# Performance work log

Measured on AMD Instinct MI355X. Metric: run time of the kernel, lower is better.

Reference implementation:

```python
import jax, jax.numpy as jnp
import numpy as np

L_SEQ = 2048
RECEPTIVE = 128  # band half-width
B, H, D = 2, 16, 64


def _band_mask(l, r, dtype):
    i = jnp.arange(l)
    return (jnp.abs(i[:, None] - i[None, :]) <= r).astype(dtype)


def setup_inputs() -> dict:
    key = jax.random.key(0)
    kq, kk = jax.random.split(key)
    queries = jax.random.normal(kq, (B, H, L_SEQ, D), dtype=jnp.float32)
    keys = jax.random.normal(kk, (B, H, L_SEQ, D), dtype=jnp.float32)
    return {"queries": queries, "keys": keys}


def reference(queries, keys):
    # Original: sum_d( q[...,i,None,d] * mask[i,j] * k[...,None,j,d] )
    # Mask is independent of d, so this equals (Q @ K^T) * band_mask.
    band = _band_mask(queries.shape[-2], RECEPTIVE, queries.dtype)  # [L, L]
    scores = jnp.einsum('bhid,bhjd->bhij', queries, keys)  # [B, H, L, L]
    return scores * band
```

## Files before the change

kernel.cpp:

```cpp
#include <hip/hip_runtime.h>


constexpr int L = 2048;
constexpr int D = 64;
constexpr int R = 128;
constexpr int TILE = 64;
constexpr int NT = L / TILE;

__global__ __launch_bounds__(256, 4)
void receptive_attention_kernel(const float* __restrict__ q,
                                const float* __restrict__ k,
                                float* __restrict__ out) {
    const int ti = blockIdx.x;
    const int y  = blockIdx.y;
    const int bh = blockIdx.z;
    const int t  = threadIdx.x;

    const int kind = (y & 1) ? (5 + (y >> 1)) : (y >> 1);

    const int jt_lo = (ti - 2 > 0) ? (ti - 2) : 0;
    const int jt_hi = (ti + 2 < NT - 1) ? (ti + 2) : (NT - 1);

    float* outStrip = out + (size_t)bh * L * L + (size_t)ti * TILE * L;

    if (kind >= 5) {
        const int r0  = (kind - 5) * 16;
        const int wl4 = (jt_lo * TILE) / 4;
        const int rb  = (jt_hi + 1) * TILE;
        const int nz4 = (L - (jt_hi - jt_lo + 1) * TILE) / 4;
        const float4 z = make_float4(0.f, 0.f, 0.f, 0.f);
        for (int r = 0; r < 16; ++r) {
            float* orow = outStrip + (size_t)(r0 + r) * L;
            for (int f = t; f < nz4; f += 256) {
                int col = (f < wl4) ? (f * 4) : (rb + (f - wl4) * 4);
                *reinterpret_cast<float4*>(orow + col) = z;
            }
        }
        return;
    }

    const int tj = ti + kind - 2;
    if (tj < 0 || tj >= NT) return;

    __shared__ __align__(16) float Qs[TILE * 64];
    __shared__ __align__(16) float Ks[TILE * 64];

    const float* qTile = q + ((size_t)bh * L + (size_t)ti * TILE) * D;
    const float* kTile = k + ((size_t)bh * L + (size_t)tj * TILE) * D;

    #pragma unroll
    for (int it = 0; it < 4; ++it) {
        int idx  = t + it * 256;
        int row  = idx >> 4;
        int col4 = idx & 15;
        float4 qv = *reinterpret_cast<const float4*>(qTile + row * D + col4 * 4);
        float4 kv = *reinterpret_cast<const float4*>(kTile + row * D + col4 * 4);
        int wblk = (col4 ^ (row >> 2)) & 15;
        *reinterpret_cast<float4*>(&Qs[row * 64 + wblk * 4]) = qv;
        *reinterpret_cast<float4*>(&Ks[row * 64 + wblk * 4]) = kv;
    }
    __syncthreads();

    const int tr = (t >> 4) * 4;
    const int tc = (t & 15) * 4;
    const int xq = (t >> 4) & 15;
    const int xk = t & 15;

    float acc[4][4] = {};
    #pragma unroll 4
    for (int b = 0; b < 16; ++b) {
        float4 qv[4], kv[4];
        const int qb = ((b ^ xq) & 15) * 4;
        const int kb = ((b ^ xk) & 15) * 4;
        #pragma unroll
        for (int r = 0; r < 4; ++r)
            qv[r] = *reinterpret_cast<const float4*>(&Qs[(tr + r) * 64 + qb]);
        #pragma unroll
        for (int c = 0; c < 4; ++c)
            kv[c] = *reinterpret_cast<const float4*>(&Ks[(tc + c) * 64 + kb]);
        #pragma unroll
        for (int rr = 0; rr < 4; ++rr) {
            #pragma unroll
            for (int cc = 0; cc < 4; ++cc) {
                acc[rr][cc] += qv[rr].x * kv[cc].x;
                acc[rr][cc] += qv[rr].y * kv[cc].y;
                acc[rr][cc] += qv[rr].z * kv[cc].z;
                acc[rr][cc] += qv[rr].w * kv[cc].w;
            }
        }
    }

    float* outTile = outStrip + tj * TILE;
    const int gi0 = ti * TILE + tr;
    const int gj0 = tj * TILE + tc;
    #pragma unroll
    for (int rr = 0; rr < 4; ++rr) {
        int gi = gi0 + rr;
        float4 v;
        float* vp = &v.x;
        #pragma unroll
        for (int cc = 0; cc < 4; ++cc) {
            int gj = gj0 + cc;
            int diff = gi - gj;
            if (diff < 0) diff = -diff;
            vp[cc] = (diff <= R) ? acc[rr][cc] : 0.f;
        }
        *reinterpret_cast<float4*>(outTile + (size_t)(tr + rr) * L + tc) = v;
    }
}

extern "C" void kernel_launch(void* const* d_in, const int* in_sizes, int n_in,
                              void* d_out, int out_size, void* d_ws, size_t ws_size,
                              hipStream_t stream) {
    const float* q = (const float*)d_in[0];
    const float* k = (const float*)d_in[1];
    float* out = (float*)d_out;

    dim3 grid(NT, 9, 32);
    receptive_attention_kernel<<<grid, 256, 0, stream>>>(q, k, out);
}
```

Measured before the change: 552.5 us.

## Merge band tiles and zero-fill into one block per row strip

Each block now handles a full 64-row output strip. It loads Q once and two warpgroups compute up to five K tiles, with K prefetched from registers into shared memory. Band results are staged in shared memory so every thread writes full-row float4 stores that cover both band and zero regions. This removes the separate zero-fill blocks and the repeated Q loads, in exchange for more syncs, higher register pressure from three accumulator sets, and a 48KB shared arena.

```diff
diff --git a/kernel.cpp b/kernel.cpp
--- a/kernel.cpp
+++ b/kernel.cpp
@@ -6,106 +6,155 @@
 constexpr int R = 128;
 constexpr int TILE = 64;
 constexpr int NT = L / TILE;
+constexpr int ARENA = 3 * TILE * 64;
 
-__global__ __launch_bounds__(256, 4)
+__global__ __launch_bounds__(512, 4)
 void receptive_attention_kernel(const float* __restrict__ q,
                                 const float* __restrict__ k,
                                 float* __restrict__ out) {
     const int ti = blockIdx.x;
-    const int y  = blockIdx.y;
-    const int bh = blockIdx.z;
+    const int bh = blockIdx.y;
     const int t  = threadIdx.x;
-
-    const int kind = (y & 1) ? (5 + (y >> 1)) : (y >> 1);
 
     const int jt_lo = (ti - 2 > 0) ? (ti - 2) : 0;
     const int jt_hi = (ti + 2 < NT - 1) ? (ti + 2) : (NT - 1);
+    const int ntj   = jt_hi - jt_lo + 1;
+    const int c0    = jt_lo * TILE;
 
-    float* outStrip = out + (size_t)bh * L * L + (size_t)ti * TILE * L;
-
-    if (kind >= 5) {
-        const int r0  = (kind - 5) * 16;
-        const int wl4 = (jt_lo * TILE) / 4;
-        const int rb  = (jt_hi + 1) * TILE;
-        const int nz4 = (L - (jt_hi - jt_lo + 1) * TILE) / 4;
-        const float4 z = make_float4(0.f, 0.f, 0.f, 0.f);
-        for (int r = 0; r < 16; ++r) {
-            float* orow = outStrip + (size_t)(r0 + r) * L;
-            for (int f = t; f < nz4; f += 256) {
-                int col = (f < wl4) ? (f * 4) : (rb + (f - wl4) * 4);
-                *reinterpret_cast<float4*>(orow + col) = z;
-            }
-        }
-        return;
-    }
-
-    const int tj = ti + kind - 2;
-    if (tj < 0 || tj >= NT) return;
-
-    __shared__ __align__(16) float Qs[TILE * 64];
-    __shared__ __align__(16) float Ks[TILE * 64];
+    __shared__ __align__(16) float smem[ARENA];
+    float* Qs = smem;
+    const int g = t >> 8;
+    const int s = t & 255;
+    float* Kg = smem + TILE * 64 + g * TILE * 64;
 
     const float* qTile = q + ((size_t)bh * L + (size_t)ti * TILE) * D;
-    const float* kTile = k + ((size_t)bh * L + (size_t)tj * TILE) * D;
+    const float* kBase = k + ((size_t)bh * L + (size_t)jt_lo * TILE) * D;
 
     #pragma unroll
-    for (int it = 0; it < 4; ++it) {
-        int idx  = t + it * 256;
+    for (int it = 0; it < 2; ++it) {
+        int idx  = t + it * 512;
         int row  = idx >> 4;
         int col4 = idx & 15;
         float4 qv = *reinterpret_cast<const float4*>(qTile + row * D + col4 * 4);
-        float4 kv = *reinterpret_cast<const float4*>(kTile + row * D + col4 * 4);
-        int wblk = (col4 ^ (row >> 2)) & 15;
-        *reinterpret_cast<float4*>(&Qs[row * 64 + wblk * 4]) = qv;
-        *reinterpret_cast<float4*>(&Ks[row * 64 + wblk * 4]) = kv;
+        int wb = (col4 ^ (row >> 2)) & 15;
+        *reinterpret_cast<float4*>(&Qs[row * 64 + wb * 4]) = qv;
+    }
+    {
+        const float* kt = kBase + (size_t)g * TILE * D;
+        #pragma unroll
+        for (int it = 0; it < 4; ++it) {
+            int idx  = s + it * 256;
+            int row  = idx >> 4;
+            int col4 = idx & 15;
+            float4 kv = *reinterpret_cast<const float4*>(kt + row * D + col4 * 4);
+            int wb = (col4 ^ (row >> 2)) & 15;
+            *reinterpret_cast<float4*>(&Kg[row * 64 + wb * 4]) = kv;
+        }
     }
     __syncthreads();
 
-    const int tr = (t >> 4) * 4;
-    const int tc = (t & 15) * 4;
-    const int xq = (t >> 4) & 15;
-    const int xk = t & 15;
+    const int tr = (s >> 4) * 4;
+    const int tc = (s & 15) * 4;
+    const int xq = (s >> 4) & 15;
+    const int xk = s & 15;
 
-    float acc[4][4] = {};
-    #pragma unroll 4
-    for (int b = 0; b < 16; ++b) {
-        float4 qv[4], kv[4];
-        const int qb = ((b ^ xq) & 15) * 4;
-        const int kb = ((b ^ xk) & 15) * 4;
-        #pragma unroll
-        for (int r = 0; r < 4; ++r)
-            qv[r] = *reinterpret_cast<const float4*>(&Qs[(tr + r) * 64 + qb]);
-        #pragma unroll
-        for (int c = 0; c < 4; ++c)
-            kv[c] = *reinterpret_cast<const float4*>(&Ks[(tc + c) * 64 + kb]);
-        #pragma unroll
-        for (int rr = 0; rr < 4; ++rr) {
-            #pragma unroll
-            for (int cc = 0; cc < 4; ++cc) {
-                acc[rr][cc] += qv[rr].x * kv[cc].x;
-                acc[rr][cc] += qv[rr].y * kv[cc].y;
-                acc[rr][cc] += qv[rr].z * kv[cc].z;
-                acc[rr][cc] += qv[rr].w * kv[cc].w;
+    float acc[3][4][4] = {};
+
+    #pragma unroll
+    for (int p = 0; p < 3; ++p) {
+        float4 nf0, nf1, nf2, nf3;
+        const int ntt = 2 * (p + 1) + g;
+        const bool npv = (p < 2) && (ntt < ntj);
+        if (npv) {
+            const float* kt = kBase + (size_t)ntt * TILE * D;
+            nf0 = *reinterpret_cast<const float4*>(kt + ((s + 0)   >> 4) * D + ((s + 0)   & 15) * 4);
+            nf1 = *reinterpret_cast<const float4*>(kt + ((s + 256) >> 4) * D + ((s + 256) & 15) * 4);
+            nf2 = *reinterpret_cast<const float4*>(kt + ((s + 512) >> 4) * D + ((s + 512) & 15) * 4);
+            nf3 = *reinterpret_cast<const float4*>(kt + ((s + 768) >> 4) * D + ((s + 768) & 15) * 4);
+        }
+
+        const int tt = 2 * p + g;
+        if (tt < ntj) {
+            #pragma unroll 4
+            for (int b = 0; b < 16; ++b) {
+                float4 qv[4], kv[4];
+                const int qb = ((b ^ xq) & 15) * 4;
+                const int kb = ((b ^ xk) & 15) * 4;
+                #pragma unroll
+                for (int r = 0; r < 4; ++r)
+                    qv[r] = *reinterpret_cast<const float4*>(&Qs[(tr + r) * 64 + qb]);
+                #pragma unroll
+                for (int c = 0; c < 4; ++c)
+                    kv[c] = *reinterpret_cast<const float4*>(&Kg[(tc + c) * 64 + kb]);
+                #pragma unroll
+                for (int rr = 0; rr < 4; ++rr) {
+                    #pragma unroll
+                    for (int cc = 0; cc < 4; ++cc) {
+                        acc[p][rr][cc] += qv[rr].x * kv[cc].x;
+                        acc[p][rr][cc] += qv[rr].y * kv[cc].y;
+                        acc[p][rr][cc] += qv[rr].z * kv[cc].z;
+                        acc[p][rr][cc] += qv[rr].w * kv[cc].w;
+                    }
+                }
             }
         }
+        __syncthreads();
+        if (npv) {
+            int r0 = (s + 0) >> 4,   c4_0 = (s + 0) & 15;
+            int r1 = (s + 256) >> 4, c4_1 = (s + 256) & 15;
+            int r2 = (s + 512) >> 4, c4_2 = (s + 512) & 15;
+            int r3 = (s + 768) >> 4, c4_3 = (s + 768) & 15;
+            *reinterpret_cast<float4*>(&Kg[r0 * 64 + (((c4_0 ^ (r0 >> 2)) & 15)) * 4]) = nf0;
+            *reinterpret_cast<float4*>(&Kg[r1 * 64 + (((c4_1 ^ (r1 >> 2)) & 15)) * 4]) = nf1;
+            *reinterpret_cast<float4*>(&Kg[r2 * 64 + (((c4_2 ^ (r2 >> 2)) & 15)) * 4]) = nf2;
+            *reinterpret_cast<float4*>(&Kg[r3 * 64 + (((c4_3 ^ (r3 >> 2)) & 15)) * 4]) = nf3;
+        }
+        __syncthreads();
     }
 
-    float* outTile = outStrip + tj * TILE;
+    float* Band = smem;
     const int gi0 = ti * TILE + tr;
-    const int gj0 = tj * TILE + tc;
+    const int bandlo4 = c0 / 4;
+    const int bandn4  = ntj * 16;
+    const int rel     = t - bandlo4;
+    float* rowBase0 = out + (size_t)bh * L * L + (size_t)ti * TILE * L;
+
     #pragma unroll
-    for (int rr = 0; rr < 4; ++rr) {
-        int gi = gi0 + rr;
-        float4 v;
-        float* vp = &v.x;
-        #pragma unroll
-        for (int cc = 0; cc < 4; ++cc) {
-            int gj = gj0 + cc;
-            int diff = gi - gj;
-            if (diff < 0) diff = -diff;
-            vp[cc] = (diff <= R) ? acc[rr][cc] : 0.f;
+    for (int half = 0; half < 2; ++half) {
+        const int rlo = half * 32;
+        if (tr >= rlo && tr < rlo + 32) {
+            #pragma unroll
+            for (int p = 0; p < 3; ++p) {
+                const int tt = 2 * p + g;
+                if (tt < ntj) {
+                    const int gj0 = (jt_lo + tt) * TILE + tc;
+                    #pragma unroll
+                    for (int rr = 0; rr < 4; ++rr) {
+                        float4 v;
+                        float* vp = &v.x;
+                        #pragma unroll
+                        for (int cc = 0; cc < 4; ++cc) {
+                            int diff = gi0 + rr - (gj0 + cc);
+                            if (diff < 0) diff = -diff;
+                            vp[cc] = (diff <= R) ? acc[p][rr][cc] : 0.f;
+                        }
+                        *reinterpret_cast<float4*>(
+                            &Band[(tr - rlo + rr) * 320 + tt * 64 + tc]) = v;
+                    }
+                }
+            }
         }
-        *reinterpret_cast<float4*>(outTile + (size_t)(tr + rr) * L + tc) = v;
+        __syncthreads();
+
+        float* rowBase = rowBase0 + (size_t)rlo * L;
+        #pragma unroll 4
+        for (int r = 0; r < 32; ++r) {
+            float4 v = make_float4(0.f, 0.f, 0.f, 0.f);
+            if (rel >= 0 && rel < bandn4)
+                v = *reinterpret_cast<float4*>(&Band[r * 320 + rel * 4]);
+            *reinterpret_cast<float4*>(rowBase + (size_t)r * L + t * 4) = v;
+        }
+        __syncthreads();
     }
 }
 
@@ -116,6 +165,6 @@
     const float* k = (const float*)d_in[1];
     float* out = (float*)d_out;
 
-    dim3 grid(NT, 9, 32);
-    receptive_attention_kernel<<<grid, 256, 0, stream>>>(q, k, out);
+    dim3 grid(NT, 32);
+    receptive_attention_kernel<<<grid, 512, 0, stream>>>(q, k, out);
 }
```

New measurement: 555.3 us. No clear change (+0.5%).
